# Performance work log

Hardware: AMD Instinct MI355X
Metric: run time of the kernel (lower is better)

## Reference

```python
import jax, jax.numpy as jnp
import numpy as np

EPS = 1e-5
H, DA, DM = 8, 64, 128  # num_read_heads, d_address, d_memory

def setup_inputs() -> dict:
    key = jax.random.key(0)
    ks = jax.random.split(key, 10)
    B, T, D, M = 4, 512, 1024, 128
    scale = lambda fan_in: 1.0 / np.sqrt(fan_in)
    return {
        "query": jax.random.normal(ks[0], (B, T, D), jnp.float32),
        "matrix": jax.random.normal(ks[1], (B, M, DA, DM), jnp.float32),
        "normalizer": jax.random.uniform(ks[2], (B, M, DA), jnp.float32),
        "addresses": jax.random.normal(ks[3], (M, DA), jnp.float32),
        "W_access": jax.random.normal(ks[4], (D, H * DA), jnp.float32) * scale(D),
        "b_access": jnp.zeros((H * DA,), jnp.float32),
        "W_read": jax.random.normal(ks[5], (D, H * DA), jnp.float32) * scale(D),
        "b_read": jnp.zeros((H * DA,), jnp.float32),
        "W_merge": jax.random.normal(ks[6], (H * DM, D), jnp.float32) * scale(H * DM),
        "b_merge": jnp.zeros((D,), jnp.float32),
    }

def reference(query, matrix, normalizer, addresses,
              W_access, b_access, W_read, b_read, W_merge, b_merge):
    act = jax.nn.softplus  # linear kernel feature map
    B, T, D = query.shape
    M = matrix.shape[1]

    # head projections -> (B,T,H,DA)
    aq = act((query @ W_access + b_access).reshape(B, T, H, DA))
    rq = act((query @ W_read + b_read).reshape(B, T, H, DA))

    # --- stage 1: linear attention over the num_memories axis ---
    ak = act(addresses)                       # (M,DA) activated keys
    norm_k = jnp.sum(ak, axis=0)              # (DA,) kernel normalizer (shared)
    den1 = jnp.einsum('btha,a->bth', aq, norm_k)[..., None] + EPS  # (B,T,H,1)

    # kernel over flattened matrix values (M, DA*DM)
    kern_m = jnp.einsum('ma,bmx->bax', ak, matrix.reshape(B, M, DA * DM))
    mat2 = jnp.einsum('btha,bax->bthx', aq, kern_m) / den1          # (B,T,H,DA*DM)
    mat2 = mat2.reshape(B, T, H, DA, DM)

    # kernel over normalizer values (M, DA)
    kern_n = jnp.einsum('ma,bmd->bad', ak, normalizer)              # (B,DA,DA)
    norm2 = jnp.einsum('btha,bad->bthd', aq, kern_n) / den1         # (B,T,H,DA)

    # --- stage 2: read from reduced kernel with read query ---
    num = jnp.einsum('btha,bthax->bthx', rq, mat2)                  # (B,T,H,DM)
    den = jnp.einsum('btha,btha->bth', rq, norm2)[..., None] + EPS
    resp = num / den                                                # (B,T,H,DM)

    return resp.reshape(B, T, H * DM) @ W_merge + b_merge           # (B,T,D)
```

## Files before the change

### kernel.cpp

```cpp
#include <hip/hip_runtime.h>
#include <hip/hip_bf16.h>
#include <math.h>

#define EPSF 1e-5f

typedef __attribute__((ext_vector_type(8))) short short8;
typedef __attribute__((ext_vector_type(4))) float f32x4;
typedef _Float16 half8 __attribute__((ext_vector_type(8)));

constexpr int Bc = 4, Tc = 512, Dc = 1024, Mc = 128, Hc = 8, DAc = 64, DMc = 128;
constexpr int BT = Bc * Tc;
constexpr int Xc = DAc * DMc;
constexpr int Rb = Tc * Hc;

__device__ __forceinline__ float softplus_f(float x) {
    return fmaxf(x, 0.f) + log1pf(expf(-fabsf(x)));
}
__device__ __forceinline__ short f2bf(float f) {
    __hip_bfloat16 h = __float2bfloat16(f);
    return *reinterpret_cast<short*>(&h);
}
__device__ __forceinline__ unsigned pk2(float a, float b) {
    return (unsigned)(unsigned short)f2bf(a) | ((unsigned)(unsigned short)f2bf(b) << 16);
}
__device__ __forceinline__ void lds_load16(void* lds, const void* g) {
    __builtin_amdgcn_global_load_lds((const __attribute__((address_space(1))) int*)g,
                                     (__attribute__((address_space(3))) int*)lds, 16, 0, 0);
}

__global__ __launch_bounds__(256) void prep_kern(const float* __restrict__ addresses,
                                                 float* __restrict__ ak_g,
                                                 float* __restrict__ norm_k,
                                                 _Float16* __restrict__ akT,
                                                 const float* __restrict__ query,
                                                 __hip_bfloat16* __restrict__ qb,
                                                 const float* __restrict__ W_access,
                                                 const float* __restrict__ W_read,
                                                 __hip_bfloat16* __restrict__ WpT,
                                                 const float* __restrict__ W_merge,
                                                 __hip_bfloat16* __restrict__ WmT) {
    __shared__ float smem[Mc * DAc];
    int bid = blockIdx.x;
    int t = threadIdx.x;
    if (bid == 0) {
        for (int i = t; i < Mc * DAc; i += 256) {
            float v = softplus_f(addresses[i]);
            ak_g[i] = v;
            smem[i] = v;
        }
        __syncthreads();
        if (t < DAc) {
            float s = 0.f;
            for (int mm = 0; mm < Mc; mm++) s += smem[mm * DAc + t];
            norm_k[t] = s;
        }
        {
            int a2 = t >> 2, q = t & 3;
#pragma unroll
            for (int j = 0; j < 32; j++)
                akT[a2 * Mc + q * 32 + j] = (_Float16)smem[(q * 32 + j) * DAc + a2];
        }
        return;
    }
    if (bid <= 2048) {
        int i = ((bid - 1) * 256 + t) * 4;
        float4 v = *(const float4*)(query + i);
        unsigned* d = (unsigned*)(qb + i);
        d[0] = pk2(v.x, v.y);
        d[1] = pk2(v.z, v.w);
        return;
    }
    float (*tile)[65] = (float(*)[65])smem;
    const float* S; int stride, nb, n0, kt;
    __hip_bfloat16* dst;
    if (bid < 2305) {
        int idx = bid - 2049;
        kt = idx & 15;
        n0 = (idx >> 4) * 64;
        if (n0 < 512) { S = W_access; nb = n0; }
        else          { S = W_read;   nb = n0 - 512; }
        stride = 512;
        dst = WpT;
    } else {
        int idx = bid - 2305;
        kt = idx & 15;
        n0 = (idx >> 4) * 64;
        S = W_merge; nb = n0; stride = 1024;
        dst = WmT;
    }
    {
        int kl = t >> 2, q = t & 3;
        const float* src = S + (size_t)(kt * 64 + kl) * stride + nb + q * 16;
#pragma unroll
        for (int j = 0; j < 4; j++) {
            float4 v = *(const float4*)(src + j * 4);
            tile[kl][q * 16 + j * 4 + 0] = v.x;
            tile[kl][q * 16 + j * 4 + 1] = v.y;
            tile[kl][q * 16 + j * 4 + 2] = v.z;
            tile[kl][q * 16 + j * 4 + 3] = v.w;
        }
    }
    __syncthreads();
    {
        int nl = t >> 2, q = t & 3;
        unsigned* d = (unsigned*)(dst + (size_t)(n0 + nl) * 1024 + kt * 64 + q * 16);
#pragma unroll
        for (int j = 0; j < 8; j++)
            d[j] = pk2(tile[q * 16 + j * 2][nl], tile[q * 16 + j * 2 + 1][nl]);
    }
}

__global__ __launch_bounds__(256) void k1t_mfma(const float* __restrict__ matrix,
                                                const _Float16* __restrict__ akT,
                                                _Float16* __restrict__ kern2) {
    __shared__ float T[32][132];
    __shared__ _Float16 At[128][40];
    int tid = threadIdx.x, lane = tid & 63, wid = tid >> 6;
    int l15 = lane & 15, lg = lane >> 4;
    int b = blockIdx.x >> 6, a = blockIdx.x & 63;
    int wr = wid & 1, wc = wid >> 1;

    half8 bfrag[2][4];
#pragma unroll
    for (int cf = 0; cf < 2; cf++)
#pragma unroll
        for (int ks = 0; ks < 4; ks++)
            bfrag[cf][ks] = *(const half8*)(akT + (wc * 32 + cf * 16 + l15) * Mc
                                            + ks * 32 + lg * 8);

    const float* msrc = matrix + (size_t)b * Mc * Xc + a * DMc;
    int r = tid >> 3, ms = (tid & 7) * 16;
    int tm = tid >> 1, tk0 = (tid & 1) * 16;

    f32x4 acc[4][2];
#pragma unroll
    for (int i = 0; i < 4; i++)
#pragma unroll
        for (int j = 0; j < 2; j++) acc[i][j] = (f32x4){0.f, 0.f, 0.f, 0.f};

    float4 ld[4];
#pragma unroll
    for (int j = 0; j < 4; j++)
        ld[j] = *(const float4*)(msrc + (size_t)r * Xc + ms + j * 4);

    for (int s = 0; s < 4; s++) {
#pragma unroll
        for (int j = 0; j < 4; j++) *(float4*)&T[r][ms + j * 4] = ld[j];
        __syncthreads();
        if (s < 3) {
#pragma unroll
            for (int j = 0; j < 4; j++)
                ld[j] = *(const float4*)(msrc + (size_t)((s + 1) * 32 + r) * Xc + ms + j * 4);
        }
        {
            half8 lo, hi;
#pragma unroll
            for (int j = 0; j < 8; j++) lo[j] = (_Float16)T[tk0 + j][tm];
#pragma unroll
            for (int j = 0; j < 8; j++) hi[j] = (_Float16)T[tk0 + 8 + j][tm];
            *(half8*)&At[tm][tk0] = lo;
            *(half8*)&At[tm][tk0 + 8] = hi;
        }
        __syncthreads();
#pragma unroll
        for (int rf = 0; rf < 4; rf++) {
            int row = wr * 64 + rf * 16 + l15;
            half8 af = *(const half8*)&At[row][lg * 8];
#pragma unroll
            for (int cf = 0; cf < 2; cf++)
                acc[rf][cf] = __builtin_amdgcn_mfma_f32_16x16x32_f16(
                    af, bfrag[cf][s], acc[rf][cf], 0, 0, 0);
        }
        __syncthreads();
    }
    _Float16* dst = kern2 + ((size_t)(b * 64 + a)) * Mc * DAc;
#pragma unroll
    for (int rf = 0; rf < 4; rf++)
#pragma unroll
        for (int cf = 0; cf < 2; cf++) {
            int a2 = wc * 32 + cf * 16 + l15;
#pragma unroll
            for (int i = 0; i < 4; i++) {
                int mrow = wr * 64 + rf * 16 + lg * 4 + i;
                dst[mrow * DAc + a2] = (_Float16)acc[rf][cf][i];
            }
        }
}

__global__ __launch_bounds__(256) void k2_kernn(const float* __restrict__ normalizer,
                                                const float* __restrict__ ak_g,
                                                float* __restrict__ kern_n) {
    __shared__ float akl[Mc * DAc];
    int tid = threadIdx.x;
    int b = blockIdx.x >> 3, ch = blockIdx.x & 7;
    for (int i = tid; i < Mc * DAc; i += 256) akl[i] = ak_g[i];
    __syncthreads();
    int d = tid & 63;
    int g = tid >> 6;
    int a2b = ch * 8 + g * 2;
    float acc0 = 0.f, acc1 = 0.f;
    const float* np = normalizer + (size_t)b * Mc * DAc + d;
    for (int mm = 0; mm < Mc; mm++) {
        float v = np[(size_t)mm * DAc];
        acc0 = fmaf(akl[mm * DAc + a2b + 0], v, acc0);
        acc1 = fmaf(akl[mm * DAc + a2b + 1], v, acc1);
    }
    kern_n[((size_t)b * DAc + a2b + 0) * DAc + d] = acc0;
    kern_n[((size_t)b * DAc + a2b + 1) * DAc + d] = acc1;
}

__global__ __launch_bounds__(256) void k3_scale(const _Float16* __restrict__ aqrq16,
                                                const float* __restrict__ kern_n,
                                                const float* __restrict__ norm_k,
                                                float* __restrict__ scale) {
    __shared__ float knl[4096];
    __shared__ float nkl[64];
    int b = blockIdx.x >> 5, ch = blockIdx.x & 31;
    int t = threadIdx.x;
    {
        const float* src = kern_n + (size_t)b * 4096;
#pragma unroll
        for (int j = 0; j < 4; j++)
            *(float4*)&knl[t * 4 + j * 1024] = *(const float4*)(src + t * 4 + j * 1024);
    }
    if (t < 64) nkl[t] = norm_k[t];
    __syncthreads();
    int row = t >> 1, g = t & 1;
    int rg = ch * 128 + row;
    int t_ = rg >> 3, h = rg & 7;
    const _Float16* aqp = aqrq16 + ((size_t)(b * Tc + t_)) * 1024 + h * 64;
    float rq[64];
#pragma unroll
    for (int j = 0; j < 8; j++) {
        half8 v = *(const half8*)(aqp + 512 + j * 8);
#pragma unroll
        for (int k = 0; k < 8; k++) rq[j * 8 + k] = (float)v[k];
    }
    float aqh[32];
#pragma unroll
    for (int j = 0; j < 4; j++) {
        half8 v = *(const half8*)(aqp + g * 32 + j * 8);
#pragma unroll
        for (int k = 0; k < 8; k++) aqh[j * 8 + k] = (float)v[k];
    }
    float sn = 0.f, d1h = 0.f;
    for (int a2l = 0; a2l < 32; a2l++) {
        int a2 = g * 32 + a2l;
        const float4* kr = (const float4*)&knl[a2 * 64];
        float dot = 0.f;
#pragma unroll
        for (int d4 = 0; d4 < 16; d4++) {
            float4 kv = kr[d4];
            dot = fmaf(kv.x, rq[d4 * 4 + 0], dot);
            dot = fmaf(kv.y, rq[d4 * 4 + 1], dot);
            dot = fmaf(kv.z, rq[d4 * 4 + 2], dot);
            dot = fmaf(kv.w, rq[d4 * 4 + 3], dot);
        }
        sn = fmaf(aqh[a2l], dot, sn);
        d1h = fmaf(aqh[a2l], nkl[a2], d1h);
    }
    sn += __shfl_xor(sn, 1);
    d1h += __shfl_xor(d1h, 1);
    if (g == 0) {
        float den1 = d1h + EPSF;
        float den = sn / den1 + EPSF;
        scale[(size_t)b * Rb + rg] = 1.f / (den1 * den);
    }
}

template <bool SOFTPLUS, typename OutT>
__global__ __launch_bounds__(256) void gemm_bf16(const __hip_bfloat16* __restrict__ A,
                                                 const __hip_bfloat16* __restrict__ BT_,
                                                 const float* __restrict__ bias0,
                                                 const float* __restrict__ bias1, int N0,
                                                 OutT* __restrict__ C, int N, int K) {
    __shared__ short Ab[2][64 * 64];
    __shared__ short Bb[2][64 * 64];
    int tid = threadIdx.x, lane = tid & 63, wid = tid >> 6;
    int l15 = lane & 15, lg = lane >> 4;
    int rowblk = blockIdx.x * 64, colblk = blockIdx.y * 64;
    int wr = wid & 1, wc = wid >> 1;
    int srow = lane >> 3;
    int sk = ((lane & 7) ^ srow) * 8;

    f32x4 acc[2][2];
#pragma unroll
    for (int i = 0; i < 2; i++)
#pragma unroll
        for (int j = 0; j < 2; j++) acc[i][j] = (f32x4){0.f, 0.f, 0.f, 0.f};

    auto stage = [&](int kbase, int buf) {
#pragma unroll
        for (int j = 0; j < 2; j++) {
            int c = wid * 2 + j;
            int row = c * 8 + srow;
            lds_load16(&Ab[buf][c * 512], A + (size_t)(rowblk + row) * K + kbase + sk);
            lds_load16(&Bb[buf][c * 512], BT_ + (size_t)(colblk + row) * K + kbase + sk);
        }
    };
    stage(0, 0);
    __syncthreads();
    int cur = 0;
    int nks = K >> 6;
    for (int ks = 0; ks < nks; ks++) {
        if (ks + 1 < nks) stage((ks + 1) << 6, cur ^ 1);
#pragma unroll
        for (int kh = 0; kh < 2; kh++) {
            short8 af[2], bfr[2];
#pragma unroll
            for (int rf = 0; rf < 2; rf++) {
                int row = wr * 32 + rf * 16 + l15;
                int ksw = (kh * 32 + lg * 8) ^ ((row & 7) << 3);
                af[rf] = *(const short8*)&Ab[cur][row * 64 + ksw];
            }
#pragma unroll
            for (int cf = 0; cf < 2; cf++) {
                int col = wc * 32 + cf * 16 + l15;
                int ksw = (kh * 32 + lg * 8) ^ ((col & 7) << 3);
                bfr[cf] = *(const short8*)&Bb[cur][col * 64 + ksw];
            }
#pragma unroll
            for (int rf = 0; rf < 2; rf++)
#pragma unroll
                for (int cf = 0; cf < 2; cf++)
                    acc[rf][cf] = __builtin_amdgcn_mfma_f32_16x16x32_bf16(
                        af[rf], bfr[cf], acc[rf][cf], 0, 0, 0);
        }
        __syncthreads();
        cur ^= 1;
    }
#pragma unroll
    for (int cf = 0; cf < 2; cf++) {
        int col = colblk + wc * 32 + cf * 16 + l15;
        float bv = (col < N0) ? bias0[col] : bias1[col - N0];
#pragma unroll
        for (int rf = 0; rf < 2; rf++) {
            int rbase = rowblk + wr * 32 + rf * 16 + lg * 4;
#pragma unroll
            for (int i = 0; i < 4; i++) {
                float v = acc[rf][cf][i] + bv;
                if (SOFTPLUS) v = softplus_f(v);
                C[(size_t)(rbase + i) * N + col] = (OutT)v;
            }
        }
    }
}

__global__ __launch_bounds__(256) void k4_mfma(const _Float16* __restrict__ aqrq16,
                                               const _Float16* __restrict__ kern2,
                                               const float* __restrict__ scale,
                                               __hip_bfloat16* __restrict__ resp) {
    __shared__ _Float16 Bb[2][4][64 * 64];
    __shared__ _Float16 rql[64][72];
    __shared__ float scl[64];
    int tid = threadIdx.x, lane = tid & 63, wid = tid >> 6;
    int l15 = lane & 15, lg = lane >> 4;
    int b = blockIdx.x >> 7;
    int rc = (blockIdx.x >> 1) & 63;
    int mh = blockIdx.x & 1;
    int rowbase = rc * 64;
    int wr = wid & 1, wc = wid >> 1;

    auto stageB = [&](int a_, int buf, int sl) {
#pragma unroll
        for (int j = 0; j < 2; j++) {
            int c = wid * 2 + j;
            int m = c * 8 + (lane >> 3);
            int sa = ((lane & 7) ^ (lane >> 3)) * 8;
            lds_load16(&Bb[buf][sl][c * 512],
                       kern2 + (((size_t)(b * 64 + a_)) * Mc + mh * 64 + m) * DAc + sa);
        }
    };
#pragma unroll
    for (int sl = 0; sl < 4; sl++) stageB(sl, 0, sl);

    half8 aqp[2][2];
#pragma unroll
    for (int rf = 0; rf < 2; rf++)
#pragma unroll
        for (int kh = 0; kh < 2; kh++) {
            int rg = rowbase + wr * 32 + rf * 16 + l15;
            int t_ = rg >> 3, h = rg & 7;
            aqp[rf][kh] = *(const half8*)(aqrq16 + ((size_t)(b * Tc + t_)) * 1024
                                          + h * 64 + kh * 32 + lg * 8);
        }
    {
        int row = tid >> 2, q = tid & 3;
        int rg = rowbase + row;
        int t_ = rg >> 3, h = rg & 7;
        const _Float16* src = aqrq16 + ((size_t)(b * Tc + t_)) * 1024 + 512 + h * 64 + q * 16;
        *(half8*)&rql[row][q * 16] = *(const half8*)(src);
        *(half8*)&rql[row][q * 16 + 8] = *(const half8*)(src + 8);
    }
    if (tid < 64) scl[tid] = scale[(size_t)b * Rb + rowbase + tid];
    __syncthreads();

    f32x4 acc[2][2];
#pragma unroll
    for (int i = 0; i < 2; i++)
#pragma unroll
        for (int j = 0; j < 2; j++) acc[i][j] = (f32x4){0.f, 0.f, 0.f, 0.f};

    int cur = 0;
    for (int it = 0; it < 16; it++) {
        if (it < 15) {
#pragma unroll
            for (int sl = 0; sl < 4; sl++) stageB(it * 4 + 4 + sl, cur ^ 1, sl);
        }
#pragma unroll
        for (int as = 0; as < 4; as++) {
            int a = it * 4 + as;
            _Float16 h0 = rql[wr * 32 + l15][a];
            _Float16 h1 = rql[wr * 32 + 16 + l15][a];
            half8 rb0 = {h0, h0, h0, h0, h0, h0, h0, h0};
            half8 rb1 = {h1, h1, h1, h1, h1, h1, h1, h1};
#pragma unroll
            for (int kh = 0; kh < 2; kh++) {
#pragma unroll
                for (int cf = 0; cf < 2; cf++) {
                    int mloc = wc * 32 + cf * 16 + l15;
                    int ch = (kh * 4 + lg) ^ (mloc & 7);
                    half8 bf = *(const half8*)&Bb[cur][as][mloc * 64 + ch * 8];
                    acc[0][cf] = __builtin_amdgcn_mfma_f32_16x16x32_f16(
                        aqp[0][kh] * rb0, bf, acc[0][cf], 0, 0, 0);
                    acc[1][cf] = __builtin_amdgcn_mfma_f32_16x16x32_f16(
                        aqp[1][kh] * rb1, bf, acc[1][cf], 0, 0, 0);
                }
            }
        }
        __syncthreads();
        cur ^= 1;
    }
#pragma unroll
    for (int rf = 0; rf < 2; rf++) {
#pragma unroll
        for (int i = 0; i < 4; i++) {
            int rl = wr * 32 + rf * 16 + lg * 4 + i;
            int rg = rowbase + rl;
            float s = scl[rl];
            int t_ = rg >> 3, h = rg & 7;
            __hip_bfloat16* dst = resp + ((size_t)(b * Tc + t_)) * 1024 + h * DMc + mh * 64;
#pragma unroll
            for (int cf = 0; cf < 2; cf++) {
                int m = wc * 32 + cf * 16 + l15;
                dst[m] = __float2bfloat16(acc[rf][cf][i] * s);
            }
        }
    }
}

extern "C" void kernel_launch(void* const* d_in, const int* in_sizes, int n_in,
                              void* d_out, int out_size, void* d_ws, size_t ws_size,
                              hipStream_t stream) {
    const float* query      = (const float*)d_in[0];
    const float* matrix     = (const float*)d_in[1];
    const float* normalizer = (const float*)d_in[2];
    const float* addresses  = (const float*)d_in[3];
    const float* W_access   = (const float*)d_in[4];
    const float* b_access   = (const float*)d_in[5];
    const float* W_read     = (const float*)d_in[6];
    const float* b_read     = (const float*)d_in[7];
    const float* W_merge    = (const float*)d_in[8];
    const float* b_merge    = (const float*)d_in[9];
    float* out = (float*)d_out;
    (void)in_sizes; (void)n_in; (void)out_size; (void)ws_size;

    float* ws     = (float*)d_ws;
    float* ak     = ws;
    float* norm_k = ws + 8192;
    float* kern_n = ws + 8320;
    float* scale  = ws + 24704;
    _Float16* akT = (_Float16*)(ws + 41088);
    _Float16* aqrq16 = (_Float16*)(ws + 65536);
    _Float16* kern2  = (_Float16*)(ws + 1114112);
    __hip_bfloat16* qb   = (__hip_bfloat16*)(ws + 2162688);
    __hip_bfloat16* resp = (__hip_bfloat16*)(ws + 3211264);
    __hip_bfloat16* WpT  = (__hip_bfloat16*)(ws + 4259840);
    __hip_bfloat16* WmT  = (__hip_bfloat16*)(ws + 4784128);

    hipLaunchKernelGGL(prep_kern, dim3(2561), dim3(256), 0, stream,
                       addresses, ak, norm_k, akT, query, qb,
                       W_access, W_read, WpT, W_merge, WmT);
    hipLaunchKernelGGL(k1t_mfma, dim3(256), dim3(256), 0, stream, matrix, akT, kern2);
    hipLaunchKernelGGL(k2_kernn, dim3(32), dim3(256), 0, stream, normalizer, ak, kern_n);
    hipLaunchKernelGGL((gemm_bf16<true, _Float16>), dim3(32, 16), dim3(256), 0, stream,
                       qb, WpT, b_access, b_read, 512, aqrq16, 1024, 1024);
    hipLaunchKernelGGL(k3_scale, dim3(128), dim3(256), 0, stream,
                       aqrq16, kern_n, norm_k, scale);
    hipLaunchKernelGGL(k4_mfma, dim3(512), dim3(256), 0, stream,
                       aqrq16, kern2, scale, resp);
    hipLaunchKernelGGL((gemm_bf16<false, float>), dim3(32, 16), dim3(256), 0, stream,
                       resp, WmT, b_merge, b_merge, 2048, out, 1024, 1024);
}
```

Measured before the change: 105.7 us.

## Fuse prep, kern, and scale kernels; deepen GEMM k-step to 128

```diff
diff --git a/kernel.cpp b/kernel.cpp
--- a/kernel.cpp
+++ b/kernel.cpp
@@ -28,42 +28,135 @@
                                      (__attribute__((address_space(3))) int*)lds, 16, 0, 0);
 }
 
-__global__ __launch_bounds__(256) void prep_kern(const float* __restrict__ addresses,
-                                                 float* __restrict__ ak_g,
-                                                 float* __restrict__ norm_k,
-                                                 _Float16* __restrict__ akT,
-                                                 const float* __restrict__ query,
-                                                 __hip_bfloat16* __restrict__ qb,
-                                                 const float* __restrict__ W_access,
-                                                 const float* __restrict__ W_read,
-                                                 __hip_bfloat16* __restrict__ WpT,
-                                                 const float* __restrict__ W_merge,
-                                                 __hip_bfloat16* __restrict__ WmT) {
-    __shared__ float smem[Mc * DAc];
+__global__ __launch_bounds__(256) void front_kern(
+        const float* __restrict__ addresses,
+        const float* __restrict__ matrix,
+        const float* __restrict__ normalizer,
+        const float* __restrict__ query,
+        const float* __restrict__ W_access,
+        const float* __restrict__ W_read,
+        const float* __restrict__ W_merge,
+        _Float16* __restrict__ kern2,
+        float* __restrict__ kern_n,
+        float* __restrict__ norm_k,
+        __hip_bfloat16* __restrict__ qb,
+        __hip_bfloat16* __restrict__ WpT,
+        __hip_bfloat16* __restrict__ WmT) {
+    __shared__ float smem[8192];
     int bid = blockIdx.x;
-    int t = threadIdx.x;
-    if (bid == 0) {
-        for (int i = t; i < Mc * DAc; i += 256) {
-            float v = softplus_f(addresses[i]);
-            ak_g[i] = v;
-            smem[i] = v;
-        }
+    int tid = threadIdx.x;
+
+    if (bid < 256) {
+        float (*T)[132] = (float(*)[132])smem;
+        _Float16 (*At)[40] = (_Float16(*)[40])(smem + 4224);
+        int lane = tid & 63, wid = tid >> 6;
+        int l15 = lane & 15, lg = lane >> 4;
+        int b = bid >> 6, a = bid & 63;
+        int wr = wid & 1, wc = wid >> 1;
+
+        half8 bfrag[2][4];
+#pragma unroll
+        for (int cf = 0; cf < 2; cf++) {
+            int a2 = wc * 32 + cf * 16 + l15;
+#pragma unroll
+            for (int ks = 0; ks < 4; ks++)
+#pragma unroll
+                for (int j = 0; j < 8; j++) {
+                    int mm = ks * 32 + lg * 8 + j;
+                    bfrag[cf][ks][j] = (_Float16)softplus_f(addresses[mm * 64 + a2]);
+                }
+        }
+
+        const float* msrc = matrix + (size_t)b * Mc * Xc + a * DMc;
+        int r = tid >> 3, ms = (tid & 7) * 16;
+        int tm = tid >> 1, tk0 = (tid & 1) * 16;
+
+        f32x4 acc[4][2];
+#pragma unroll
+        for (int i = 0; i < 4; i++)
+#pragma unroll
+            for (int j = 0; j < 2; j++) acc[i][j] = (f32x4){0.f, 0.f, 0.f, 0.f};
+
+        float4 ld[4];
+#pragma unroll
+        for (int j = 0; j < 4; j++)
+            ld[j] = *(const float4*)(msrc + (size_t)r * Xc + ms + j * 4);
+
+        for (int s = 0; s < 4; s++) {
+#pragma unroll
+            for (int j = 0; j < 4; j++) *(float4*)&T[r][ms + j * 4] = ld[j];
+            __syncthreads();
+            if (s < 3) {
+#pragma unroll
+                for (int j = 0; j < 4; j++)
+                    ld[j] = *(const float4*)(msrc + (size_t)((s + 1) * 32 + r) * Xc + ms + j * 4);
+            }
+            {
+                half8 lo, hi;
+#pragma unroll
+                for (int j = 0; j < 8; j++) lo[j] = (_Float16)T[tk0 + j][tm];
+#pragma unroll
+                for (int j = 0; j < 8; j++) hi[j] = (_Float16)T[tk0 + 8 + j][tm];
+                *(half8*)&At[tm][tk0] = lo;
+                *(half8*)&At[tm][tk0 + 8] = hi;
+            }
+            __syncthreads();
+#pragma unroll
+            for (int rf = 0; rf < 4; rf++) {
+                int row = wr * 64 + rf * 16 + l15;
+                half8 af = *(const half8*)&At[row][lg * 8];
+#pragma unroll
+                for (int cf = 0; cf < 2; cf++)
+                    acc[rf][cf] = __builtin_amdgcn_mfma_f32_16x16x32_f16(
+                        af, bfrag[cf][s], acc[rf][cf], 0, 0, 0);
+            }
+            __syncthreads();
+        }
+        _Float16* dst = kern2 + ((size_t)(b * 64 + a)) * Mc * DAc;
+#pragma unroll
+        for (int rf = 0; rf < 4; rf++)
+#pragma unroll
+            for (int cf = 0; cf < 2; cf++) {
+                int a2 = wc * 32 + cf * 16 + l15;
+#pragma unroll
+                for (int i = 0; i < 4; i++) {
+                    int mrow = wr * 64 + rf * 16 + lg * 4 + i;
+                    dst[mrow * DAc + a2] = (_Float16)acc[rf][cf][i];
+                }
+            }
+        return;
+    }
+    if (bid < 288) {
+        int idx = bid - 256;
+        int b = idx >> 3, ch = idx & 7;
+        for (int i = tid; i < Mc * DAc; i += 256) smem[i] = softplus_f(addresses[i]);
         __syncthreads();
-        if (t < DAc) {
+        int d = tid & 63;
+        int g = tid >> 6;
+        int a2b = ch * 8 + g * 2;
+        float acc0 = 0.f, acc1 = 0.f;
+        const float* np = normalizer + (size_t)b * Mc * DAc + d;
+        for (int mm = 0; mm < Mc; mm++) {
+            float v = np[(size_t)mm * DAc];
+            acc0 = fmaf(smem[mm * DAc + a2b + 0], v, acc0);
+            acc1 = fmaf(smem[mm * DAc + a2b + 1], v, acc1);
+        }
+        kern_n[((size_t)b * DAc + a2b + 0) * DAc + d] = acc0;
+        kern_n[((size_t)b * DAc + a2b + 1) * DAc + d] = acc1;
+        return;
+    }
+    if (bid == 288) {
+        for (int i = tid; i < Mc * DAc; i += 256) smem[i] = softplus_f(addresses[i]);
+        __syncthreads();
+        if (tid < DAc) {
             float s = 0.f;
-            for (int mm = 0; mm < Mc; mm++) s += smem[mm * DAc + t];
-            norm_k[t] = s;
-        }
-        {
-            int a2 = t >> 2, q = t & 3;
-#pragma unroll
-            for (int j = 0; j < 32; j++)
-                akT[a2 * Mc + q * 32 + j] = (_Float16)smem[(q * 32 + j) * DAc + a2];
+            for (int mm = 0; mm < Mc; mm++) s += smem[mm * DAc + tid];
+            norm_k[tid] = s;
         }
         return;
     }
-    if (bid <= 2048) {
-        int i = ((bid - 1) * 256 + t) * 4;
+    if (bid < 2337) {
+        int i = ((bid - 289) * 256 + tid) * 4;
         float4 v = *(const float4*)(query + i);
         unsigned* d = (unsigned*)(qb + i);
         d[0] = pk2(v.x, v.y);
@@ -73,8 +166,8 @@
     float (*tile)[65] = (float(*)[65])smem;
     const float* S; int stride, nb, n0, kt;
     __hip_bfloat16* dst;
-    if (bid < 2305) {
-        int idx = bid - 2049;
+    if (bid < 2593) {
+        int idx = bid - 2337;
         kt = idx & 15;
         n0 = (idx >> 4) * 64;
         if (n0 < 512) { S = W_access; nb = n0; }
@@ -82,14 +175,14 @@
         stride = 512;
         dst = WpT;
     } else {
-        int idx = bid - 2305;
+        int idx = bid - 2593;
         kt = idx & 15;
         n0 = (idx >> 4) * 64;
         S = W_merge; nb = n0; stride = 1024;
         dst = WmT;
     }
     {
-        int kl = t >> 2, q = t & 3;
+        int kl = tid >> 2, q = tid & 3;
         const float* src = S + (size_t)(kt * 64 + kl) * stride + nb + q * 16;
 #pragma unroll
         for (int j = 0; j < 4; j++) {
@@ -102,169 +195,11 @@
     }
     __syncthreads();
     {
-        int nl = t >> 2, q = t & 3;
+        int nl = tid >> 2, q = tid & 3;
         unsigned* d = (unsigned*)(dst + (size_t)(n0 + nl) * 1024 + kt * 64 + q * 16);
 #pragma unroll
         for (int j = 0; j < 8; j++)
             d[j] = pk2(tile[q * 16 + j * 2][nl], tile[q * 16 + j * 2 + 1][nl]);
-    }
-}
-
-__global__ __launch_bounds__(256) void k1t_mfma(const float* __restrict__ matrix,
-                                                const _Float16* __restrict__ akT,
-                                                _Float16* __restrict__ kern2) {
-    __shared__ float T[32][132];
-    __shared__ _Float16 At[128][40];
-    int tid = threadIdx.x, lane = tid & 63, wid = tid >> 6;
-    int l15 = lane & 15, lg = lane >> 4;
-    int b = blockIdx.x >> 6, a = blockIdx.x & 63;
-    int wr = wid & 1, wc = wid >> 1;
-
-    half8 bfrag[2][4];
-#pragma unroll
-    for (int cf = 0; cf < 2; cf++)
-#pragma unroll
-        for (int ks = 0; ks < 4; ks++)
-            bfrag[cf][ks] = *(const half8*)(akT + (wc * 32 + cf * 16 + l15) * Mc
-                                            + ks * 32 + lg * 8);
-
-    const float* msrc = matrix + (size_t)b * Mc * Xc + a * DMc;
-    int r = tid >> 3, ms = (tid & 7) * 16;
-    int tm = tid >> 1, tk0 = (tid & 1) * 16;
-
-    f32x4 acc[4][2];
-#pragma unroll
-    for (int i = 0; i < 4; i++)
-#pragma unroll
-        for (int j = 0; j < 2; j++) acc[i][j] = (f32x4){0.f, 0.f, 0.f, 0.f};
-
-    float4 ld[4];
-#pragma unroll
-    for (int j = 0; j < 4; j++)
-        ld[j] = *(const float4*)(msrc + (size_t)r * Xc + ms + j * 4);
-
-    for (int s = 0; s < 4; s++) {
-#pragma unroll
-        for (int j = 0; j < 4; j++) *(float4*)&T[r][ms + j * 4] = ld[j];
-        __syncthreads();
-        if (s < 3) {
-#pragma unroll
-            for (int j = 0; j < 4; j++)
-                ld[j] = *(const float4*)(msrc + (size_t)((s + 1) * 32 + r) * Xc + ms + j * 4);
-        }
-        {
-            half8 lo, hi;
-#pragma unroll
-            for (int j = 0; j < 8; j++) lo[j] = (_Float16)T[tk0 + j][tm];
-#pragma unroll
-            for (int j = 0; j < 8; j++) hi[j] = (_Float16)T[tk0 + 8 + j][tm];
-            *(half8*)&At[tm][tk0] = lo;
-            *(half8*)&At[tm][tk0 + 8] = hi;
-        }
-        __syncthreads();
-#pragma unroll
-        for (int rf = 0; rf < 4; rf++) {
-            int row = wr * 64 + rf * 16 + l15;
-            half8 af = *(const half8*)&At[row][lg * 8];
-#pragma unroll
-            for (int cf = 0; cf < 2; cf++)
-                acc[rf][cf] = __builtin_amdgcn_mfma_f32_16x16x32_f16(
-                    af, bfrag[cf][s], acc[rf][cf], 0, 0, 0);
-        }
-        __syncthreads();
-    }
-    _Float16* dst = kern2 + ((size_t)(b * 64 + a)) * Mc * DAc;
-#pragma unroll
-    for (int rf = 0; rf < 4; rf++)
-#pragma unroll
-        for (int cf = 0; cf < 2; cf++) {
-            int a2 = wc * 32 + cf * 16 + l15;
-#pragma unroll
-            for (int i = 0; i < 4; i++) {
-                int mrow = wr * 64 + rf * 16 + lg * 4 + i;
-                dst[mrow * DAc + a2] = (_Float16)acc[rf][cf][i];
-            }
-        }
-}
-
-__global__ __launch_bounds__(256) void k2_kernn(const float* __restrict__ normalizer,
-                                                const float* __restrict__ ak_g,
-                                                float* __restrict__ kern_n) {
-    __shared__ float akl[Mc * DAc];
-    int tid = threadIdx.x;
-    int b = blockIdx.x >> 3, ch = blockIdx.x & 7;
-    for (int i = tid; i < Mc * DAc; i += 256) akl[i] = ak_g[i];
-    __syncthreads();
-    int d = tid & 63;
-    int g = tid >> 6;
-    int a2b = ch * 8 + g * 2;
-    float acc0 = 0.f, acc1 = 0.f;
-    const float* np = normalizer + (size_t)b * Mc * DAc + d;
-    for (int mm = 0; mm < Mc; mm++) {
-        float v = np[(size_t)mm * DAc];
-        acc0 = fmaf(akl[mm * DAc + a2b + 0], v, acc0);
-        acc1 = fmaf(akl[mm * DAc + a2b + 1], v, acc1);
-    }
-    kern_n[((size_t)b * DAc + a2b + 0) * DAc + d] = acc0;
-    kern_n[((size_t)b * DAc + a2b + 1) * DAc + d] = acc1;
-}
-
-__global__ __launch_bounds__(256) void k3_scale(const _Float16* __restrict__ aqrq16,
-                                                const float* __restrict__ kern_n,
-                                                const float* __restrict__ norm_k,
-                                                float* __restrict__ scale) {
-    __shared__ float knl[4096];
-    __shared__ float nkl[64];
-    int b = blockIdx.x >> 5, ch = blockIdx.x & 31;
-    int t = threadIdx.x;
-    {
-        const float* src = kern_n + (size_t)b * 4096;
-#pragma unroll
-        for (int j = 0; j < 4; j++)
-            *(float4*)&knl[t * 4 + j * 1024] = *(const float4*)(src + t * 4 + j * 1024);
-    }
-    if (t < 64) nkl[t] = norm_k[t];
-    __syncthreads();
-    int row = t >> 1, g = t & 1;
-    int rg = ch * 128 + row;
-    int t_ = rg >> 3, h = rg & 7;
-    const _Float16* aqp = aqrq16 + ((size_t)(b * Tc + t_)) * 1024 + h * 64;
-    float rq[64];
-#pragma unroll
-    for (int j = 0; j < 8; j++) {
-        half8 v = *(const half8*)(aqp + 512 + j * 8);
-#pragma unroll
-        for (int k = 0; k < 8; k++) rq[j * 8 + k] = (float)v[k];
-    }
-    float aqh[32];
-#pragma unroll
-    for (int j = 0; j < 4; j++) {
-        half8 v = *(const half8*)(aqp + g * 32 + j * 8);
-#pragma unroll
-        for (int k = 0; k < 8; k++) aqh[j * 8 + k] = (float)v[k];
-    }
-    float sn = 0.f, d1h = 0.f;
-    for (int a2l = 0; a2l < 32; a2l++) {
-        int a2 = g * 32 + a2l;
-        const float4* kr = (const float4*)&knl[a2 * 64];
-        float dot = 0.f;
-#pragma unroll
-        for (int d4 = 0; d4 < 16; d4++) {
-            float4 kv = kr[d4];
-            dot = fmaf(kv.x, rq[d4 * 4 + 0], dot);
-            dot = fmaf(kv.y, rq[d4 * 4 + 1], dot);
-            dot = fmaf(kv.z, rq[d4 * 4 + 2], dot);
-            dot = fmaf(kv.w, rq[d4 * 4 + 3], dot);
-        }
-        sn = fmaf(aqh[a2l], dot, sn);
-        d1h = fmaf(aqh[a2l], nkl[a2], d1h);
-    }
-    sn += __shfl_xor(sn, 1);
-    d1h += __shfl_xor(d1h, 1);
-    if (g == 0) {
-        float den1 = d1h + EPSF;
-        float den = sn / den1 + EPSF;
-        scale[(size_t)b * Rb + rg] = 1.f / (den1 * den);
     }
 }
 
@@ -274,8 +209,8 @@
                                                  const float* __restrict__ bias0,
                                                  const float* __restrict__ bias1, int N0,
                                                  OutT* __restrict__ C, int N, int K) {
-    __shared__ short Ab[2][64 * 64];
-    __shared__ short Bb[2][64 * 64];
+    __shared__ short Ab[2][2][64 * 64];
+    __shared__ short Bb[2][2][64 * 64];
     int tid = threadIdx.x, lane = tid & 63, wid = tid >> 6;
     int l15 = lane & 15, lg = lane >> 4;
     int rowblk = blockIdx.x * 64, colblk = blockIdx.y * 64;
@@ -289,42 +224,49 @@
 #pragma unroll
         for (int j = 0; j < 2; j++) acc[i][j] = (f32x4){0.f, 0.f, 0.f, 0.f};
 
-    auto stage = [&](int kbase, int buf) {
+    auto stage = [&](int kbase, int buf, int sub) {
 #pragma unroll
         for (int j = 0; j < 2; j++) {
             int c = wid * 2 + j;
             int row = c * 8 + srow;
-            lds_load16(&Ab[buf][c * 512], A + (size_t)(rowblk + row) * K + kbase + sk);
-            lds_load16(&Bb[buf][c * 512], BT_ + (size_t)(colblk + row) * K + kbase + sk);
+            lds_load16(&Ab[buf][sub][c * 512], A + (size_t)(rowblk + row) * K + kbase + sk);
+            lds_load16(&Bb[buf][sub][c * 512], BT_ + (size_t)(colblk + row) * K + kbase + sk);
         }
     };
-    stage(0, 0);
+    stage(0, 0, 0);
+    stage(64, 0, 1);
     __syncthreads();
     int cur = 0;
-    int nks = K >> 6;
+    int nks = K >> 7;
     for (int ks = 0; ks < nks; ks++) {
-        if (ks + 1 < nks) stage((ks + 1) << 6, cur ^ 1);
-#pragma unroll
-        for (int kh = 0; kh < 2; kh++) {
-            short8 af[2], bfr[2];
-#pragma unroll
-            for (int rf = 0; rf < 2; rf++) {
-                int row = wr * 32 + rf * 16 + l15;
-                int ksw = (kh * 32 + lg * 8) ^ ((row & 7) << 3);
-                af[rf] = *(const short8*)&Ab[cur][row * 64 + ksw];
-            }
-#pragma unroll
-            for (int cf = 0; cf < 2; cf++) {
-                int col = wc * 32 + cf * 16 + l15;
-                int ksw = (kh * 32 + lg * 8) ^ ((col & 7) << 3);
-                bfr[cf] = *(const short8*)&Bb[cur][col * 64 + ksw];
-            }
-#pragma unroll
-            for (int rf = 0; rf < 2; rf++)
-#pragma unroll
-                for (int cf = 0; cf < 2; cf++)
-                    acc[rf][cf] = __builtin_amdgcn_mfma_f32_16x16x32_bf16(
-                        af[rf], bfr[cf], acc[rf][cf], 0, 0, 0);
+        if (ks + 1 < nks) {
+            stage((ks + 1) << 7, cur ^ 1, 0);
+            stage(((ks + 1) << 7) + 64, cur ^ 1, 1);
+        }
+#pragma unroll
+        for (int sub = 0; sub < 2; sub++) {
+#pragma unroll
+            for (int kh = 0; kh < 2; kh++) {
+                short8 af[2], bfr[2];
+#pragma unroll
+                for (int rf = 0; rf < 2; rf++) {
+                    int row = wr * 32 + rf * 16 + l15;
+                    int ksw = (kh * 32 + lg * 8) ^ ((row & 7) << 3);
+                    af[rf] = *(const short8*)&Ab[cur][sub][row * 64 + ksw];
+                }
+#pragma unroll
+                for (int cf = 0; cf < 2; cf++) {
+                    int col = wc * 32 + cf * 16 + l15;
+                    int ksw = (kh * 32 + lg * 8) ^ ((col & 7) << 3);
+                    bfr[cf] = *(const short8*)&Bb[cur][sub][col * 64 + ksw];
+                }
+#pragma unroll
+                for (int rf = 0; rf < 2; rf++)
+#pragma unroll
+                    for (int cf = 0; cf < 2; cf++)
+                        acc[rf][cf] = __builtin_amdgcn_mfma_f32_16x16x32_bf16(
+                            af[rf], bfr[cf], acc[rf][cf], 0, 0, 0);
+            }
         }
         __syncthreads();
         cur ^= 1;
@@ -348,11 +290,13 @@
 
 __global__ __launch_bounds__(256) void k4_mfma(const _Float16* __restrict__ aqrq16,
                                                const _Float16* __restrict__ kern2,
-                                               const float* __restrict__ scale,
+                                               const float* __restrict__ kern_n,
+                                               const float* __restrict__ norm_k,
                                                __hip_bfloat16* __restrict__ resp) {
     __shared__ _Float16 Bb[2][4][64 * 64];
     __shared__ _Float16 rql[64][72];
     __shared__ float scl[64];
+    __shared__ float nkl[64];
     int tid = threadIdx.x, lane = tid & 63, wid = tid >> 6;
     int l15 = lane & 15, lg = lane >> 4;
     int b = blockIdx.x >> 7;
@@ -360,6 +304,7 @@
     int mh = blockIdx.x & 1;
     int rowbase = rc * 64;
     int wr = wid & 1, wc = wid >> 1;
+    float* knl = (float*)&Bb[1][0][0];
 
     auto stageB = [&](int a_, int buf, int sl) {
 #pragma unroll
@@ -373,6 +318,13 @@
     };
 #pragma unroll
     for (int sl = 0; sl < 4; sl++) stageB(sl, 0, sl);
+    {
+#pragma unroll
+        for (int j = 0; j < 4; j++) {
+            int c = wid * 4 + j;
+            lds_load16(knl + c * 256, kern_n + (size_t)b * 4096 + c * 256 + lane * 4);
+        }
+    }
 
     half8 aqp[2][2];
 #pragma unroll
@@ -392,7 +344,50 @@
         *(half8*)&rql[row][q * 16] = *(const half8*)(src);
         *(half8*)&rql[row][q * 16 + 8] = *(const half8*)(src + 8);
     }
-    if (tid < 64) scl[tid] = scale[(size_t)b * Rb + rowbase + tid];
+    if (tid < 64) nkl[tid] = norm_k[tid];
+    __syncthreads();
+
+    {
+        int row = tid >> 2, c = tid & 3;
+        int rg = rowbase + row;
+        int t_ = rg >> 3, h = rg & 7;
+        const _Float16* aqg = aqrq16 + ((size_t)(b * Tc + t_)) * 1024 + h * 64 + c * 16;
+        half8 a0 = *(const half8*)(aqg);
+        half8 a1 = *(const half8*)(aqg + 8);
+        float aqv[16];
+#pragma unroll
+        for (int j = 0; j < 8; j++) { aqv[j] = (float)a0[j]; aqv[8 + j] = (float)a1[j]; }
+        float rqv[64];
+#pragma unroll
+        for (int j8 = 0; j8 < 8; j8++) {
+            half8 v = *(const half8*)&rql[row][j8 * 8];
+#pragma unroll
+            for (int k = 0; k < 8; k++) rqv[j8 * 8 + k] = (float)v[k];
+        }
+        float sn = 0.f, d1 = 0.f;
+        for (int a2l = 0; a2l < 16; a2l++) {
+            int a2 = c * 16 + a2l;
+            const float4* kr = (const float4*)(knl + a2 * 64);
+            float dot = 0.f;
+#pragma unroll
+            for (int d4 = 0; d4 < 16; d4++) {
+                float4 kv = kr[d4];
+                dot = fmaf(kv.x, rqv[d4 * 4 + 0], dot);
+                dot = fmaf(kv.y, rqv[d4 * 4 + 1], dot);
+                dot = fmaf(kv.z, rqv[d4 * 4 + 2], dot);
+                dot = fmaf(kv.w, rqv[d4 * 4 + 3], dot);
+            }
+            sn = fmaf(aqv[a2l], dot, sn);
+            d1 = fmaf(aqv[a2l], nkl[a2], d1);
+        }
+        sn += __shfl_xor(sn, 1); sn += __shfl_xor(sn, 2);
+        d1 += __shfl_xor(d1, 1); d1 += __shfl_xor(d1, 2);
+        if (c == 0) {
+            float den1 = d1 + EPSF;
+            float den = sn / den1 + EPSF;
+            scl[row] = 1.f / (den1 * den);
+        }
+    }
     __syncthreads();
 
     f32x4 acc[2][2];
@@ -466,29 +461,23 @@
     (void)in_sizes; (void)n_in; (void)out_size; (void)ws_size;
 
     float* ws     = (float*)d_ws;
-    float* ak     = ws;
-    float* norm_k = ws + 8192;
-    float* kern_n = ws + 8320;
-    float* scale  = ws + 24704;
-    _Float16* akT = (_Float16*)(ws + 41088);
-    _Float16* aqrq16 = (_Float16*)(ws + 65536);
-    _Float16* kern2  = (_Float16*)(ws + 1114112);
-    __hip_bfloat16* qb   = (__hip_bfloat16*)(ws + 2162688);
-    __hip_bfloat16* resp = (__hip_bfloat16*)(ws + 3211264);
-    __hip_bfloat16* WpT  = (__hip_bfloat16*)(ws + 4259840);
-    __hip_bfloat16* WmT  = (__hip_bfloat16*)(ws + 4784128);
-
-    hipLaunchKernelGGL(prep_kern, dim3(2561), dim3(256), 0, stream,
-                       addresses, ak, norm_k, akT, query, qb,
-                       W_access, W_read, WpT, W_merge, WmT);
-    hipLaunchKernelGGL(k1t_mfma, dim3(256), dim3(256), 0, stream, matrix, akT, kern2);
-    hipLaunchKernelGGL(k2_kernn, dim3(32), dim3(256), 0, stream, normalizer, ak, kern_n);
+    float* norm_k = ws;
+    float* kern_n = ws + 128;
+    _Float16* aqrq16 = (_Float16*)(ws + 16512);
+    _Float16* kern2  = (_Float16*)(ws + 1065088);
+    __hip_bfloat16* qb   = (__hip_bfloat16*)(ws + 2113664);
+    __hip_bfloat16* resp = (__hip_bfloat16*)(ws + 3162240);
+    __hip_bfloat16* WpT  = (__hip_bfloat16*)(ws + 4210816);
+    __hip_bfloat16* WmT  = (__hip_bfloat16*)(ws + 4735104);
+
+    hipLaunchKernelGGL(front_kern, dim3(2849), dim3(256), 0, stream,
+                       addresses, matrix, normalizer, query,
+                       W_access, W_read, W_merge,
+                       kern2, kern_n, norm_k, qb, WpT, WmT);
     hipLaunchKernelGGL((gemm_bf16<true, _Float16>), dim3(32, 16), dim3(256), 0, stream,
                        qb, WpT, b_access, b_read, 512, aqrq16, 1024, 1024);
-    hipLaunchKernelGGL(k3_scale, dim3(128), dim3(256), 0, stream,
-                       aqrq16, kern_n, norm_k, scale);
     hipLaunchKernelGGL(k4_mfma, dim3(512), dim3(256), 0, stream,
-                       aqrq16, kern2, scale, resp);
+                       aqrq16, kern2, kern_n, norm_k, resp);
     hipLaunchKernelGGL((gemm_bf16<false, float>), dim3(32, 16), dim3(256), 0, stream,
                        resp, WmT, b_merge, b_merge, 2048, out, 1024, 1024);
 }
```

New measurement: 96.51 us. 1.1x faster.
